# Performance work log

Measured on AMD Instinct MI355X. Metric: run time of the kernel, lower is better.

Reference implementation:

```python
import jax, jax.numpy as jnp
import numpy as np

N_LAYERS = 4
D = 512
H = 8
DH = D // H
DFF = 2048
VOCAB = 32000
SEQ_LEN = 512
MEM_LEN = 512
CMEM_LEN = 128
RATIO = 4
SCALE = DH ** -0.5


def _ln(x, g, b, eps=1e-5):
    mu = x.mean(-1, keepdims=True)
    var = ((x - mu) ** 2).mean(-1, keepdims=True)
    return (x - mu) * jax.lax.rsqrt(var + eps) * g + b


def _pe(t, d):
    # sinusoidal positional encoding buffer (PositionalEncoding)
    pos = np.arange(t, dtype=np.float32)[:, None]
    div = np.exp(np.arange(0, d, 2, dtype=np.float32) * (-np.log(10000.0) / d))
    pe = np.zeros((t, d), np.float32)
    pe[:, 0::2] = np.sin(pos * div)
    pe[:, 1::2] = np.cos(pos * div)
    return jnp.asarray(pe)


def _heads(x):  # [b,l,d] -> [b,h,l,dh]
    b, l, _ = x.shape
    return x.reshape(b, l, H, DH).transpose(0, 2, 1, 3)


def _full_attn(q, k, v):
    dots = jnp.einsum('bhid,bhjd->bhij', q, k) * SCALE
    return jnp.einsum('bhij,bhjd->bhid', jax.nn.softmax(dots, -1), v)


def _forward(seq, mask, mems, cmems, embed, ln1_g, ln1_b, Wq, Wkv, Wo, bo,
             conv_w, conv_b, ln2_g, ln2_b, W1, b1, W2, b2):
    b, t = seq.shape
    x = embed[seq] + _pe(t, D)[None]  # embedding + positional encoding
    # 2-D input mask -> [b,1,t,mem+cmem+t], True on memory positions
    mm = mask[:, None, :, None] & mask[:, None, None, :]
    full_mask = jnp.pad(mm, ((0, 0), (0, 0), (0, 0), (MEM_LEN + CMEM_LEN, 0)),
                        constant_values=True)
    neg = -jnp.finfo(jnp.float32).max
    new_mems, new_cmems, attns = [], [], []
    aux_total = jnp.zeros((), jnp.float32)
    for i in range(N_LAYERS):
        # PreNorm -> MemoryMultiHeadedAttention -> Residual
        xn = _ln(x, ln1_g[i], ln1_b[i])
        q = _heads(xn @ Wq[i])
        kv_in = jnp.concatenate([cmems[i], mems[i], xn], axis=1)  # [b,cm+m+t,d]
        k, v = jnp.split(kv_in @ Wkv[i], 2, axis=-1)
        k, v = _heads(k), _heads(v)
        dots = jnp.einsum('bhid,bhjd->bhij', q, k) * SCALE
        dots = jnp.where(full_mask, dots, neg)
        attn = jax.nn.softmax(dots, -1)
        out = jnp.einsum('bhij,bhjd->bhid', attn, v).transpose(0, 2, 1, 3).reshape(b, t, D)
        x = out @ Wo[i] + bo[i] + x  # to_out + residual
        # FIFO memory update: queue (mem, xn), keep last MEM_LEN
        queue = jnp.concatenate([mems[i], xn], axis=1)
        old_mem, new_mem = queue[:, :-MEM_LEN], queue[:, -MEM_LEN:]
        # ConvCompress with stride==kernel==RATIO -> non-overlapping blocks
        blocks = old_mem.reshape(b, -1, RATIO, D)
        compressed = jnp.einsum('birc,ocr->bio', blocks, conv_w[i]) + conv_b[i]
        new_cmem = jnp.concatenate([cmems[i], compressed], axis=1)[:, -CMEM_LEN:]
        # reconstruction attention loss; all operands detached as in source
        ck, cv = jnp.split(compressed @ Wkv[i], 2, axis=-1)
        qd, okd, ovd, ckd, cvd = map(jax.lax.stop_gradient, (
            q,
            k[:, :, CMEM_LEN:CMEM_LEN + MEM_LEN],
            v[:, :, CMEM_LEN:CMEM_LEN + MEM_LEN],
            _heads(ck), _heads(cv)))
        aux_total = aux_total + jnp.mean((_full_attn(qd, okd, ovd) - _full_attn(qd, ckd, cvd)) ** 2)
        # PreNorm -> FeedForward(GELU) -> Residual
        xn2 = _ln(x, ln2_g[i], ln2_b[i])
        x = x + jax.nn.gelu(xn2 @ W1[i] + b1[i], approximate=False) @ W2[i] + b2[i]
        new_mems.append(new_mem)
        new_cmems.append(new_cmem)
        attns.append(attn)
    attns_mean = jnp.mean(jnp.stack(attns), axis=(0, 1, 2))  # [t, cm+m+t]
    return (x, jnp.stack(new_mems), jnp.stack(new_cmems),
            aux_total / N_LAYERS, jnp.zeros((), jnp.float32), attns_mean)


def setup_inputs():
    key = jax.random.key(0)
    ks = jax.random.split(key, 12)
    s = 0.02
    return {
        'seq': jax.random.randint(ks[0], (8, SEQ_LEN), 0, VOCAB),
        'mask': jnp.ones((8, SEQ_LEN), bool),
        'mems': jax.random.normal(ks[1], (N_LAYERS, 8, MEM_LEN, D), jnp.float32) * s,
        'cmems': jax.random.normal(ks[2], (N_LAYERS, 8, CMEM_LEN, D), jnp.float32) * s,
        'embed': jax.random.normal(ks[3], (VOCAB, D), jnp.float32) * s,
        'ln1_g': jnp.ones((N_LAYERS, D)), 'ln1_b': jnp.zeros((N_LAYERS, D)),
        'Wq': jax.random.normal(ks[4], (N_LAYERS, D, D), jnp.float32) * s,
        'Wkv': jax.random.normal(ks[5], (N_LAYERS, D, 2 * D), jnp.float32) * s,
        'Wo': jax.random.normal(ks[6], (N_LAYERS, D, D), jnp.float32) * s,
        'bo': jnp.zeros((N_LAYERS, D)),
        'conv_w': jax.random.normal(ks[7], (N_LAYERS, D, D, RATIO), jnp.float32) * s,
        'conv_b': jnp.zeros((N_LAYERS, D)),
        'ln2_g': jnp.ones((N_LAYERS, D)), 'ln2_b': jnp.zeros((N_LAYERS, D)),
        'W1': jax.random.normal(ks[8], (N_LAYERS, D, DFF), jnp.float32) * s,
        'b1': jnp.zeros((N_LAYERS, DFF)),
        'W2': jax.random.normal(ks[9], (N_LAYERS, DFF, D), jnp.float32) * s,
        'b2': jnp.zeros((N_LAYERS, D)),
    }


def reference(seq, mask, mems, cmems, embed, ln1_g, ln1_b, Wq, Wkv, Wo, bo,
              conv_w, conv_b, ln2_g, ln2_b, W1, b1, W2, b2):
    return _forward(seq, mask, mems, cmems, embed, ln1_g, ln1_b, Wq, Wkv, Wo, bo,
                    conv_w, conv_b, ln2_g, ln2_b, W1, b1, W2, b2)
```

## Files before the change

### kernel.cpp

```cpp
#include <hip/hip_runtime.h>
#include <hip/hip_bf16.h>

#define DEV __device__ __forceinline__

typedef unsigned short u16;
typedef __attribute__((ext_vector_type(8))) short short8;
typedef __attribute__((ext_vector_type(4))) float floatx4;

DEV float gelu_f(float x){ return 0.5f*x*(1.0f+erff(x*0.7071067811865476f)); }

DEV u16 f2bf(float x){
  union { __hip_bfloat16 h; u16 u; } cv;
  cv.h = __float2bfloat16(x);
  return cv.u;
}
DEV float bf2f(u16 u){
  union { unsigned int u32; float f; } cv;
  cv.u32 = ((unsigned int)u) << 16;
  return cv.f;
}
DEV void split2(float v, u16* H, u16* L, long long i){
  u16 h = f2bf(v); H[i] = h; L[i] = f2bf(v - bf2f(h));
}

DEV void stage16(const u16* g, u16* lwave, int lane){
#if __has_builtin(__builtin_amdgcn_global_load_lds)
  __builtin_amdgcn_global_load_lds((const __attribute__((address_space(1))) void*)g,
                                   (__attribute__((address_space(3))) void*)lwave, 16, 0, 0);
#else
  *(short8*)(lwave + (long long)lane*8) = *(const short8*)g;
#endif
}

DEV float blockReduceSum(float v){
  __shared__ float red[4];
  int lane = threadIdx.x & 63, wid = threadIdx.x >> 6;
  #pragma unroll
  for (int off=32; off>0; off>>=1) v += __shfl_down(v, off, 64);
  __syncthreads();
  if (lane==0) red[wid]=v;
  __syncthreads();
  return red[0]+red[1]+red[2]+red[3];
}
DEV float blockReduceMax(float v){
  __shared__ float redm[4];
  int lane = threadIdx.x & 63, wid = threadIdx.x >> 6;
  #pragma unroll
  for (int off=32; off>0; off>>=1) v = fmaxf(v, __shfl_down(v, off, 64));
  __syncthreads();
  if (lane==0) redm[wid]=v;
  __syncthreads();
  return fmaxf(fmaxf(redm[0],redm[1]),fmaxf(redm[2],redm[3]));
}

template<int BM, int BN>
__global__ __launch_bounds__(256) void mgemm(
    const u16* __restrict__ AH, const u16* __restrict__ AL,
    const u16* __restrict__ BH, const u16* __restrict__ BL,
    float* __restrict__ C, u16* __restrict__ CH, u16* __restrict__ CL,
    const float* __restrict__ bias, const float* __restrict__ resid,
    float* __restrict__ mirror,
    int K, int lda, int ldb, int ldc,
    long long sA1, long long sA2, long long sB1, long long sB2,
    long long sC1, long long sC2, int B2, float scale, int act)
{
  const int b1 = blockIdx.z / B2, b2 = blockIdx.z % B2;
  const long long aOff = b1*sA1 + b2*sA2;
  const long long bOff = b1*sB1 + b2*sB2;
  const long long cOff = b1*sC1 + b2*sC2;
  AH += aOff; AL += aOff; BH += bOff; BL += bOff;
  if (C) C += cOff;
  if (CH){ CH += cOff; CL += cOff; }
  if (resid) resid += cOff;
  if (mirror) mirror += cOff;

  const int m0 = blockIdx.y*BM, n0 = blockIdx.x*BN;
  const int tid = threadIdx.x, lane = tid & 63, wid = tid >> 6;
  const int ln15 = lane & 15, quad = lane >> 4;
  constexpr int WM = BM/2, WN = BN/2, FM = WM/16, FN = WN/16;
  constexpr int RWA = BM/4, RWB = BN/4;
  constexpr int NIA = BM/64, NIB = BN/64;
  const int wr = wid >> 1, wc = wid & 1;

  __shared__ u16 AsH[2*BM*32];
  __shared__ u16 AsL[2*BM*32];
  __shared__ u16 BsH[2*BN*32];
  __shared__ u16 BsL[2*BN*32];

  floatx4 acc[FM][FN];
  #pragma unroll
  for (int a=0;a<FM;++a)
    #pragma unroll
    for (int b=0;b<FN;++b) acc[a][b] = (floatx4){0.f,0.f,0.f,0.f};

  const int rA = wid*RWA + (lane >> 2), cA = (lane & 3)*8;
  const int rB = wid*RWB + (lane >> 2), cB = (lane & 3)*8;
  const u16* pAH = AH + (long long)(m0 + rA)*lda + cA;
  const u16* pAL = AL + (long long)(m0 + rA)*lda + cA;
  const u16* pBH = BH + (long long)(n0 + rB)*ldb + cB;
  const u16* pBL = BL + (long long)(n0 + rB)*ldb + cB;
  u16* lAH = &AsH[wid*RWA*32];
  u16* lAL = &AsL[wid*RWA*32];
  u16* lBH = &BsH[wid*RWB*32];
  u16* lBL = &BsL[wid*RWB*32];

  for (int k0 = 0; k0 < K; k0 += 64) {
    #pragma unroll
    for (int s=0;s<2;++s){
      #pragma unroll
      for (int j=0;j<NIA;++j){
        stage16(pAH + s*32 + (long long)j*16*lda, lAH + s*BM*32 + j*512, lane);
        stage16(pAL + s*32 + (long long)j*16*lda, lAL + s*BM*32 + j*512, lane);
      }
      #pragma unroll
      for (int j=0;j<NIB;++j){
        stage16(pBH + s*32 + (long long)j*16*ldb, lBH + s*BN*32 + j*512, lane);
        stage16(pBL + s*32 + (long long)j*16*ldb, lBL + s*BN*32 + j*512, lane);
      }
    }
    __syncthreads();

    short8 ah[FM][2], al[FM][2], bh[FN][2], bl[FN][2];
    #pragma unroll
    for (int mi=0; mi<FM; ++mi)
      #pragma unroll
      for (int s=0;s<2;++s){
        const int off = s*BM*32 + (wr*WM + mi*16 + ln15)*32 + quad*8;
        ah[mi][s] = *(const short8*)&AsH[off];
        al[mi][s] = *(const short8*)&AsL[off];
      }
    #pragma unroll
    for (int ni=0; ni<FN; ++ni)
      #pragma unroll
      for (int s=0;s<2;++s){
        const int off = s*BN*32 + (wc*WN + ni*16 + ln15)*32 + quad*8;
        bh[ni][s] = *(const short8*)&BsH[off];
        bl[ni][s] = *(const short8*)&BsL[off];
      }
    #pragma unroll
    for (int mi=0; mi<FM; ++mi)
      #pragma unroll
      for (int ni=0; ni<FN; ++ni){
        floatx4 c = acc[mi][ni];
        #pragma unroll
        for (int s=0;s<2;++s){
          c = __builtin_amdgcn_mfma_f32_16x16x32_bf16(ah[mi][s], bh[ni][s], c, 0,0,0);
          c = __builtin_amdgcn_mfma_f32_16x16x32_bf16(ah[mi][s], bl[ni][s], c, 0,0,0);
          c = __builtin_amdgcn_mfma_f32_16x16x32_bf16(al[mi][s], bh[ni][s], c, 0,0,0);
        }
        acc[mi][ni] = c;
      }
    __syncthreads();
    pAH += 64; pAL += 64; pBH += 64; pBL += 64;
  }

  #pragma unroll
  for (int mi=0; mi<FM; ++mi){
    const int rb = m0 + wr*WM + mi*16 + quad*4;
    #pragma unroll
    for (int ni=0; ni<FN; ++ni){
      const int col = n0 + wc*WN + ni*16 + ln15;
      const float bv = bias ? bias[col] : 0.f;
      #pragma unroll
      for (int r=0; r<4; ++r){
        const long long ci = (long long)(rb+r)*ldc + col;
        float v = acc[mi][ni][r]*scale + bv;
        if (act==1) v = gelu_f(v);
        if (resid) v += resid[ci];
        if (C) C[ci] = v;
        if (CH){ u16 h=f2bf(v); CH[ci]=h; CL[ci]=f2bf(v-bf2f(h)); }
        if (mirror) mirror[ci] = v;
      }
    }
  }
}

__global__ __launch_bounds__(256) void wtrans_split(
    const float* __restrict__ W, u16* __restrict__ WTH, u16* __restrict__ WTL,
    int K, int N)
{
  __shared__ float t[32][33];
  const int k0 = blockIdx.x*32, n0 = blockIdx.y*32;
  const int r = threadIdx.x >> 5, c = threadIdx.x & 31;
  #pragma unroll
  for (int p=0;p<4;++p) t[r+p*8][c] = W[(long long)(k0+r+p*8)*N + n0+c];
  __syncthreads();
  #pragma unroll
  for (int p=0;p<4;++p){
    const float v = t[c][r+p*8];
    split2(v, WTH, WTL, (long long)(n0+r+p*8)*K + k0+c);
  }
}

__global__ __launch_bounds__(256) void wpermT_split(
    const float* __restrict__ w, u16* __restrict__ H, u16* __restrict__ L)
{
  const int idx = blockIdx.x*256 + threadIdx.x;
  const int o = idx >> 11, rem = idx & 2047;
  const int r = rem >> 9, c = rem & 511;
  split2(w[(long long)o*2048 + c*4 + r], H, L, idx);
}

__global__ __launch_bounds__(256) void vtrans_hl(
    const u16* __restrict__ kvH, const u16* __restrict__ kvL,
    u16* __restrict__ vTH, u16* __restrict__ vTL)
{
  const int z = blockIdx.y, t0 = blockIdx.x*64;
  const int b = z >> 3, h = z & 7;
  __shared__ u16 tH[64][72], tL[64][72];
  const int r = threadIdx.x >> 6, c = threadIdx.x & 63;
  #pragma unroll
  for (int p=0;p<16;++p){
    const int row = r + p*4;
    const long long off = (long long)b*1179648 + (long long)(t0+row)*1024 + 512 + h*64 + c;
    tH[row][c] = kvH[off];
    tL[row][c] = kvL[off];
  }
  __syncthreads();
  #pragma unroll
  for (int p=0;p<16;++p){
    const int d = r + p*4;
    const long long o = (long long)z*73728 + (long long)d*1152 + t0 + c;
    vTH[o] = tH[c][d];
    vTL[o] = tL[c][d];
  }
}

__global__ __launch_bounds__(256) void cvtrans_hl(
    const u16* __restrict__ ckvH, const u16* __restrict__ ckvL,
    u16* __restrict__ cvTH, u16* __restrict__ cvTL)
{
  const int z = blockIdx.y, t0 = blockIdx.x*64;
  const int b = z >> 3, h = z & 7;
  __shared__ u16 tH[64][72], tL[64][72];
  const int r = threadIdx.x >> 6, c = threadIdx.x & 63;
  #pragma unroll
  for (int p=0;p<16;++p){
    const int row = r + p*4;
    const long long off = (long long)b*131072 + (long long)(t0+row)*1024 + 512 + h*64 + c;
    tH[row][c] = ckvH[off];
    tL[row][c] = ckvL[off];
  }
  __syncthreads();
  #pragma unroll
  for (int p=0;p<16;++p){
    const int d = r + p*4;
    const long long o = (long long)z*8192 + (long long)d*128 + t0 + c;
    cvTH[o] = tH[c][d];
    cvTL[o] = tL[c][d];
  }
}

__global__ __launch_bounds__(256) void embed_kernel(
    const int* __restrict__ seq, const float* __restrict__ emb,
    float* __restrict__ x)
{
  const int row = blockIdx.x;
  const int t = row & 511;
  const long long tok = seq[row];
  #pragma unroll
  for (int p = 0; p < 2; ++p) {
    const int d = threadIdx.x + p*256;
    const int j2 = d & ~1;
    const float div = __expf((float)j2 * (-0.0179889460f));
    const float ang = (float)t * div;
    const float pe = (d & 1) ? cosf(ang) : sinf(ang);
    x[(long long)row*512 + d] = emb[tok*512 + d] + pe;
  }
}

__global__ __launch_bounds__(256) void ln_kernel(
    const float* __restrict__ x, const float* __restrict__ g,
    const float* __restrict__ b, u16* __restrict__ outH, u16* __restrict__ outL,
    float* __restrict__ mirror)
{
  const long long base = (long long)blockIdx.x*512;
  const int tid = threadIdx.x;
  const float v0 = x[base+tid], v1 = x[base+tid+256];
  const float mean = blockReduceSum(v0+v1) * (1.f/512.f);
  const float d0 = v0-mean, d1 = v1-mean;
  const float var = blockReduceSum(d0*d0+d1*d1) * (1.f/512.f);
  const float rstd = rsqrtf(var + 1e-5f);
  const float o0 = d0*rstd*g[tid]     + b[tid];
  const float o1 = d1*rstd*g[tid+256] + b[tid+256];
  split2(o0, outH, outL, base+tid);
  split2(o1, outH, outL, base+tid+256);
  if (mirror) { mirror[base+tid] = o0; mirror[base+tid+256] = o1; }
}

__global__ __launch_bounds__(256) void build_cm_kernel(
    const float* __restrict__ cmems_i, const float* __restrict__ mems_i,
    u16* __restrict__ H, u16* __restrict__ L)
{
  const long long idx = (long long)blockIdx.x*256 + threadIdx.x;
  const int c = (int)(idx & 511);
  const long long rb = idx >> 9;
  const int r = (int)(rb % 640);
  const int b = (int)(rb / 640);
  float v;
  if (r < 128) v = cmems_i[(long long)b*65536 + (long long)r*512 + c];
  else         v = mems_i[(long long)b*262144 + (long long)(r-128)*512 + c];
  split2(v, H, L, idx);
}

template<int MAXP>
__global__ __launch_bounds__(256) void softmax_hl(
    u16* __restrict__ H, u16* __restrict__ L, int Wd, float* __restrict__ acc)
{
  const long long base = (long long)blockIdx.x * Wd;
  float v[MAXP];
  float mx = -3.4e38f;
  #pragma unroll
  for (int p = 0; p < MAXP; ++p){
    const int i = threadIdx.x + p*256;
    v[p] = (i < Wd) ? bf2f(H[base+i]) + bf2f(L[base+i]) : -3.4e38f;
    mx = fmaxf(mx, v[p]);
  }
  mx = blockReduceMax(mx);
  float sum = 0.f;
  #pragma unroll
  for (int p = 0; p < MAXP; ++p){
    const int i = threadIdx.x + p*256;
    if (i < Wd){ v[p] = __expf(v[p] - mx); sum += v[p]; }
  }
  sum = blockReduceSum(sum);
  const float inv = 1.f/sum;
  float* arow = acc ? acc + (long long)(blockIdx.x & 511)*Wd : nullptr;
  #pragma unroll
  for (int p = 0; p < MAXP; ++p){
    const int i = threadIdx.x + p*256;
    if (i < Wd){
      const float e = v[p]*inv;
      split2(e, H, L, base+i);
      if (arow) atomicAdd(arow + i, e);
    }
  }
}

__global__ __launch_bounds__(256) void sqdiff_kernel(
    const float* __restrict__ a, const float* __restrict__ b, float* __restrict__ accum)
{
  const int idx0 = blockIdx.x*1024 + threadIdx.x;
  float s = 0.f;
  #pragma unroll
  for (int p = 0; p < 4; ++p) {
    const int idx = idx0 + p*256;
    const float d = a[idx]-b[idx];
    s += d*d;
  }
  s = blockReduceSum(s);
  if (threadIdx.x == 0) atomicAdd(accum, s);
}

__global__ __launch_bounds__(256) void attns_final_kernel(
    const float* __restrict__ asum, float* __restrict__ out)
{
  const int idx = blockIdx.x*256 + threadIdx.x;
  if (idx < 589824) out[idx] = asum[idx]*(1.f/256.f);
}

__global__ void aux_final_kernel(const float* __restrict__ aux, float* __restrict__ out)
{
  out[0] = aux[0] * (1.f/8388608.f);
  out[1] = 0.f;
}

extern "C" void kernel_launch(void* const* d_in, const int* in_sizes, int n_in,
                              void* d_out, int out_size, void* d_ws, size_t ws_size,
                              hipStream_t stream)
{
  const int*   seq    = (const int*)d_in[0];
  const float* mems   = (const float*)d_in[2];
  const float* cmems  = (const float*)d_in[3];
  const float* embed  = (const float*)d_in[4];
  const float* ln1_g  = (const float*)d_in[5];
  const float* ln1_b  = (const float*)d_in[6];
  const float* Wq     = (const float*)d_in[7];
  const float* Wkv    = (const float*)d_in[8];
  const float* Wo     = (const float*)d_in[9];
  const float* bo     = (const float*)d_in[10];
  const float* conv_w = (const float*)d_in[11];
  const float* conv_b = (const float*)d_in[12];
  const float* ln2_g  = (const float*)d_in[13];
  const float* ln2_b  = (const float*)d_in[14];
  const float* W1     = (const float*)d_in[15];
  const float* b1     = (const float*)d_in[16];
  const float* W2     = (const float*)d_in[17];
  const float* b2     = (const float*)d_in[18];
  float* out = (float*)d_out;

  char* W8 = (char*)d_ws;
  float* x     = (float*)(W8 + 0);
  u16* xnH     = (u16*)(W8 + 8388608LL);
  u16* xnL     = (u16*)(W8 + 12582912LL);
  u16* qH      = (u16*)(W8 + 16777216LL);
  u16* qL      = (u16*)(W8 + 20971520LL);
  u16* cmH     = (u16*)(W8 + 25165824LL);
  u16* cmL     = (u16*)(W8 + 30408704LL);
  u16* kvH     = (u16*)(W8 + 35651584LL);
  u16* kvL     = (u16*)(W8 + 54525952LL);
  u16* vTH     = (u16*)(W8 + 73400320LL);
  u16* vTL     = (u16*)(W8 + 82837504LL);
  u16* dotsH   = (u16*)(W8 + 92274688LL);
  u16* dotsL   = (u16*)(W8 + 111149056LL);
  u16* aoutH   = (u16*)(W8 + 130023424LL);
  u16* aoutL   = (u16*)(W8 + 134217728LL);
  u16* compH   = (u16*)(W8 + 138412032LL);
  u16* compL   = (u16*)(W8 + 139460608LL);
  u16* ckvH    = (u16*)(W8 + 140509184LL);
  u16* ckvL    = (u16*)(W8 + 142606336LL);
  u16* cvTH    = (u16*)(W8 + 144703488LL);
  u16* cvTL    = (u16*)(W8 + 145752064LL);
  u16* wpTH    = (u16*)(W8 + 146800640LL);
  u16* wpTL    = (u16*)(W8 + 148897792LL);
  u16* WqTH    = (u16*)(W8 + 150994944LL);
  u16* WqTL    = (u16*)(W8 + 151519232LL);
  u16* WkvTH   = (u16*)(W8 + 152043520LL);
  u16* WkvTL   = (u16*)(W8 + 153092096LL);
  u16* WoTH    = (u16*)(W8 + 154140672LL);
  u16* WoTL    = (u16*)(W8 + 154664960LL);
  u16* W1TH    = (u16*)(W8 + 155189248LL);
  u16* W1TL    = (u16*)(W8 + 157286400LL);
  u16* W2TH    = (u16*)(W8 + 159383552LL);
  u16* W2TL    = (u16*)(W8 + 161480704LL);
  float* o1    = (float*)(W8 + 163577856LL);
  float* o2    = (float*)(W8 + 171966464LL);
  float* attns = (float*)(W8 + 180355072LL);
  float* aux   = (float*)(W8 + 182714368LL);
  u16* xn2H = qH;  u16* xn2L = qL;
  u16* ffnhH = kvH; u16* ffnhL = kvL;

  hipMemsetAsync(attns, 0, 589824*sizeof(float), stream);
  hipMemsetAsync(aux, 0, sizeof(float), stream);

  embed_kernel<<<4096,256,0,stream>>>(seq, embed, x);

  for (int i = 0; i < 4; ++i) {
    const float* bo_i   = bo   + (long long)i*512;
    const float* cw_i   = conv_w + (long long)i*1048576;
    const float* cb_i   = conv_b + (long long)i*512;
    const float* b1_i   = b1   + (long long)i*2048;
    const float* b2_i   = b2   + (long long)i*512;
    const float* mems_i = mems + (long long)i*2097152;
    const float* cmems_i= cmems+ (long long)i*524288;
    float* out_mems_i   = out + 2097152LL  + (long long)i*2097152;
    float* out_cmems_i  = out + 10485760LL + (long long)i*524288;

    wtrans_split<<<dim3(16,16),256,0,stream>>>(Wq + (long long)i*262144,  WqTH, WqTL, 512, 512);
    wtrans_split<<<dim3(16,32),256,0,stream>>>(Wkv+ (long long)i*524288,  WkvTH,WkvTL,512, 1024);
    wtrans_split<<<dim3(16,16),256,0,stream>>>(Wo + (long long)i*262144,  WoTH, WoTL, 512, 512);
    wtrans_split<<<dim3(16,64),256,0,stream>>>(W1 + (long long)i*1048576, W1TH, W1TL, 512, 2048);
    wtrans_split<<<dim3(64,16),256,0,stream>>>(W2 + (long long)i*1048576, W2TH, W2TL, 2048,512);

    ln_kernel<<<4096,256,0,stream>>>(x, ln1_g+(long long)i*512, ln1_b+(long long)i*512, xnH, xnL, out_mems_i);
    mgemm<64,64><<<dim3(8,64,1),256,0,stream>>>(
        xnH,xnL, WqTH,WqTL, nullptr, qH,qL, nullptr,nullptr,nullptr,
        512, 512,512,512, 0,0,0,0,0,0, 1, 1.f, 0);
    build_cm_kernel<<<10240,256,0,stream>>>(cmems_i, mems_i, cmH, cmL);
    mgemm<64,128><<<dim3(8,10,8),256,0,stream>>>(
        cmH,cmL, WkvTH,WkvTL, nullptr, kvH,kvL, nullptr,nullptr,nullptr,
        512, 512,512,1024, 0,327680, 0,0, 0,1179648, 8, 1.f, 0);
    mgemm<64,128><<<dim3(8,8,8),256,0,stream>>>(
        xnH,xnL, WkvTH,WkvTL, nullptr, kvH+655360,kvL+655360, nullptr,nullptr,nullptr,
        512, 512,512,1024, 0,262144, 0,0, 0,1179648, 8, 1.f, 0);
    vtrans_hl<<<dim3(18,64),256,0,stream>>>(kvH, kvL, vTH, vTL);
    for (int c = 0; c < 4; ++c) {
      mgemm<64,128><<<dim3(9,8,16),256,0,stream>>>(
          qH + (long long)c*524288, qL + (long long)c*524288,
          kvH + (long long)c*2359296, kvL + (long long)c*2359296,
          nullptr, dotsH, dotsL, nullptr,nullptr,nullptr,
          64, 512,1024,1152, 262144,64, 1179648,64, 4718592,589824, 8, 0.125f, 0);
      softmax_hl<5><<<8192,256,0,stream>>>(dotsH, dotsL, 1152, attns);
      mgemm<64,64><<<dim3(1,8,16),256,0,stream>>>(
          dotsH, dotsL, vTH + (long long)c*1179648, vTL + (long long)c*1179648,
          nullptr, aoutH + (long long)c*524288, aoutL + (long long)c*524288,
          nullptr,nullptr,nullptr,
          1152, 1152,1152,512, 4718592,589824, 589824,73728, 262144,64, 8, 1.f, 0);
    }
    mgemm<64,64><<<dim3(8,64,1),256,0,stream>>>(
        aoutH,aoutL, WoTH,WoTL, x, nullptr,nullptr, bo_i, x, nullptr,
        512, 512,512,512, 0,0,0,0,0,0, 1, 1.f, 0);
    wpermT_split<<<4096,256,0,stream>>>(cw_i, wpTH, wpTL);
    mgemm<64,64><<<dim3(8,2,8),256,0,stream>>>(
        cmH+65536, cmL+65536, wpTH, wpTL, out_cmems_i, compH, compL, cb_i, nullptr, nullptr,
        2048, 2048,2048,512, 0,327680, 0,0, 0,65536, 8, 1.f, 0);
    mgemm<64,64><<<dim3(16,16,1),256,0,stream>>>(
        compH,compL, WkvTH,WkvTL, nullptr, ckvH,ckvL, nullptr,nullptr,nullptr,
        512, 512,512,1024, 0,0,0,0,0,0, 1, 1.f, 0);
    cvtrans_hl<<<dim3(2,64),256,0,stream>>>(ckvH, ckvL, cvTH, cvTL);
    for (int c = 0; c < 4; ++c) {
      mgemm<64,128><<<dim3(4,8,16),256,0,stream>>>(
          qH + (long long)c*524288, qL + (long long)c*524288,
          kvH + (long long)c*2359296 + 131072, kvL + (long long)c*2359296 + 131072,
          nullptr, dotsH, dotsL, nullptr,nullptr,nullptr,
          64, 512,1024,512, 262144,64, 1179648,64, 2097152,262144, 8, 0.125f, 0);
      softmax_hl<2><<<8192,256,0,stream>>>(dotsH, dotsL, 512, nullptr);
      mgemm<64,64><<<dim3(1,8,16),256,0,stream>>>(
          dotsH, dotsL, vTH + (long long)c*1179648 + 128, vTL + (long long)c*1179648 + 128,
          o1 + (long long)c*524288, nullptr,nullptr, nullptr,nullptr,nullptr,
          512, 512,1152,64, 2097152,262144, 589824,73728, 262144,32768, 8, 1.f, 0);
    }
    mgemm<64,128><<<dim3(1,8,64),256,0,stream>>>(
        qH,qL, ckvH,ckvL, nullptr, dotsH, dotsL, nullptr,nullptr,nullptr,
        64, 512,1024,128, 262144,64, 131072,64, 524288,65536, 8, 0.125f, 0);
    softmax_hl<1><<<32768,256,0,stream>>>(dotsH, dotsL, 128, nullptr);
    mgemm<64,64><<<dim3(1,8,64),256,0,stream>>>(
        dotsH, dotsL, cvTH, cvTL, o2, nullptr,nullptr, nullptr,nullptr,nullptr,
        128, 128,128,64, 524288,65536, 65536,8192, 262144,32768, 8, 1.f, 0);
    sqdiff_kernel<<<2048,256,0,stream>>>(o1, o2, aux);
    ln_kernel<<<4096,256,0,stream>>>(x, ln2_g+(long long)i*512, ln2_b+(long long)i*512, xn2H, xn2L, nullptr);
    mgemm<64,128><<<dim3(16,64,1),256,0,stream>>>(
        xn2H,xn2L, W1TH,W1TL, nullptr, ffnhH,ffnhL, b1_i, nullptr, nullptr,
        512, 512,512,2048, 0,0,0,0,0,0, 1, 1.f, 1);
    mgemm<64,64><<<dim3(8,64,1),256,0,stream>>>(
        ffnhH,ffnhL, W2TH,W2TL, x, nullptr,nullptr, b2_i, x, (i==3) ? out : nullptr,
        2048, 2048,2048,512, 0,0,0,0,0,0, 1, 1.f, 0);
  }

  attns_final_kernel<<<2304,256,0,stream>>>(attns, out + 12582914LL);
  aux_final_kernel<<<1,1,0,stream>>>(aux, out + 12582912LL);
}
```

Baseline: 3.539 ms.

## Fuse memory attention QK, softmax and PV into a two-pass flash kernel

Replaces the per-chunk sequence of QK^T GEMM, split-precision softmax and PV GEMM with a single fused attention kernel. A first pass computes running row max and sum over the 1152 keys; a second pass recomputes the scores, normalizes them, accumulates the attention map with atomics and multiplies by V from shared memory. This avoids writing and re-reading the large hi/lo score buffers and cuts several launches per layer. In exchange it computes QK twice and does many float atomicAdds into the attention map.

```diff
diff --git a/kernel.cpp b/kernel.cpp
--- a/kernel.cpp
+++ b/kernel.cpp
@@ -171,6 +171,201 @@
         if (CH){ u16 h=f2bf(v); CH[ci]=h; CL[ci]=f2bf(v-bf2f(h)); }
         if (mirror) mirror[ci] = v;
       }
+    }
+  }
+}
+
+__global__ __launch_bounds__(256) void fattn(
+    const u16* __restrict__ qH_, const u16* __restrict__ qL_,
+    const u16* __restrict__ kvH_, const u16* __restrict__ kvL_,
+    const u16* __restrict__ vTH_, const u16* __restrict__ vTL_,
+    u16* __restrict__ aoH, u16* __restrict__ aoL,
+    float* __restrict__ attns)
+{
+  const int z = blockIdx.y, b = z >> 3, h = z & 7;
+  const int t0 = blockIdx.x * 64;
+  const int tid = threadIdx.x, lane = tid & 63, wid = tid >> 6;
+  const int ln15 = lane & 15, quad = lane >> 4;
+
+  __shared__ u16 QsH[4096], QsL[4096], KsH[4096], KsL[4096];
+  __shared__ u16 VsH[4096], VsL[4096], PsH[4096], PsL[4096];
+
+  const int rS = wid*16 + (lane >> 2), cS = (lane & 3)*8;
+
+  {
+    const u16* qh = qH_ + (long long)(b*512 + t0 + rS)*512 + h*64 + cS;
+    const u16* ql = qL_ + (long long)(b*512 + t0 + rS)*512 + h*64 + cS;
+    stage16(qh,    &QsH[wid*512], lane);
+    stage16(qh+32, &QsH[2048 + wid*512], lane);
+    stage16(ql,    &QsL[wid*512], lane);
+    stage16(ql+32, &QsL[2048 + wid*512], lane);
+  }
+  const u16* kHb = kvH_ + (long long)b*1179648 + h*64;
+  const u16* kLb = kvL_ + (long long)b*1179648 + h*64;
+  const u16* vHb = vTH_ + (long long)z*73728;
+  const u16* vLb = vTL_ + (long long)z*73728;
+  __syncthreads();
+
+  short8 qfh[2], qfl[2];
+  #pragma unroll
+  for (int s=0;s<2;++s){
+    const int off = s*2048 + (wid*16 + ln15)*32 + quad*8;
+    qfh[s] = *(const short8*)&QsH[off];
+    qfl[s] = *(const short8*)&QsL[off];
+  }
+
+  float m_run[4] = {-3.4e38f,-3.4e38f,-3.4e38f,-3.4e38f};
+  float l_run[4] = {0.f,0.f,0.f,0.f};
+
+  for (int tt = 0; tt < 1152; tt += 64) {
+    __syncthreads();
+    {
+      const u16* kh = kHb + (long long)(tt + rS)*1024 + cS;
+      const u16* kl = kLb + (long long)(tt + rS)*1024 + cS;
+      stage16(kh,    &KsH[wid*512], lane);
+      stage16(kh+32, &KsH[2048 + wid*512], lane);
+      stage16(kl,    &KsL[wid*512], lane);
+      stage16(kl+32, &KsL[2048 + wid*512], lane);
+    }
+    __syncthreads();
+
+    short8 kh[4][2], kl[4][2];
+    #pragma unroll
+    for (int ni=0;ni<4;++ni)
+      #pragma unroll
+      for (int s=0;s<2;++s){
+        const int off = s*2048 + (ni*16 + ln15)*32 + quad*8;
+        kh[ni][s] = *(const short8*)&KsH[off];
+        kl[ni][s] = *(const short8*)&KsL[off];
+      }
+    floatx4 acc[4];
+    #pragma unroll
+    for (int ni=0;ni<4;++ni){
+      floatx4 c = (floatx4){0.f,0.f,0.f,0.f};
+      #pragma unroll
+      for (int s=0;s<2;++s){
+        c = __builtin_amdgcn_mfma_f32_16x16x32_bf16(qfh[s], kh[ni][s], c, 0,0,0);
+        c = __builtin_amdgcn_mfma_f32_16x16x32_bf16(qfh[s], kl[ni][s], c, 0,0,0);
+        c = __builtin_amdgcn_mfma_f32_16x16x32_bf16(qfl[s], kh[ni][s], c, 0,0,0);
+      }
+      acc[ni] = c;
+    }
+    #pragma unroll
+    for (int r=0;r<4;++r){
+      float v = fmaxf(fmaxf(acc[0][r],acc[1][r]),fmaxf(acc[2][r],acc[3][r]));
+      #pragma unroll
+      for (int o=1;o<16;o<<=1) v = fmaxf(v, __shfl_xor(v, o, 64));
+      const float mn = fmaxf(m_run[r], 0.125f*v);
+      float sum = 0.f;
+      #pragma unroll
+      for (int ni=0;ni<4;++ni) sum += __expf(0.125f*acc[ni][r] - mn);
+      #pragma unroll
+      for (int o=1;o<16;o<<=1) sum += __shfl_xor(sum, o, 64);
+      l_run[r] = l_run[r]*__expf(m_run[r]-mn) + sum;
+      m_run[r] = mn;
+    }
+  }
+  float invl[4];
+  #pragma unroll
+  for (int r=0;r<4;++r) invl[r] = 1.f/l_run[r];
+
+  floatx4 o_acc[4];
+  #pragma unroll
+  for (int ni=0;ni<4;++ni) o_acc[ni] = (floatx4){0.f,0.f,0.f,0.f};
+
+  for (int tt = 0; tt < 1152; tt += 64) {
+    __syncthreads();
+    {
+      const u16* kh = kHb + (long long)(tt + rS)*1024 + cS;
+      const u16* kl = kLb + (long long)(tt + rS)*1024 + cS;
+      stage16(kh,    &KsH[wid*512], lane);
+      stage16(kh+32, &KsH[2048 + wid*512], lane);
+      stage16(kl,    &KsL[wid*512], lane);
+      stage16(kl+32, &KsL[2048 + wid*512], lane);
+    }
+    __syncthreads();
+
+    short8 kh[4][2], kl[4][2];
+    #pragma unroll
+    for (int ni=0;ni<4;++ni)
+      #pragma unroll
+      for (int s=0;s<2;++s){
+        const int off = s*2048 + (ni*16 + ln15)*32 + quad*8;
+        kh[ni][s] = *(const short8*)&KsH[off];
+        kl[ni][s] = *(const short8*)&KsL[off];
+      }
+    floatx4 acc[4];
+    #pragma unroll
+    for (int ni=0;ni<4;++ni){
+      floatx4 c = (floatx4){0.f,0.f,0.f,0.f};
+      #pragma unroll
+      for (int s=0;s<2;++s){
+        c = __builtin_amdgcn_mfma_f32_16x16x32_bf16(qfh[s], kh[ni][s], c, 0,0,0);
+        c = __builtin_amdgcn_mfma_f32_16x16x32_bf16(qfh[s], kl[ni][s], c, 0,0,0);
+        c = __builtin_amdgcn_mfma_f32_16x16x32_bf16(qfl[s], kh[ni][s], c, 0,0,0);
+      }
+      acc[ni] = c;
+    }
+    const int rowl = wid*16 + quad*4;
+    #pragma unroll
+    for (int ni=0;ni<4;++ni){
+      const int cl = ln15 + ni*16;
+      const int soff = (cl>>5)*2048 + (cl&31);
+      #pragma unroll
+      for (int r=0;r<4;++r){
+        const float p = __expf(0.125f*acc[ni][r] - m_run[r])*invl[r];
+        atomicAdd(&attns[(long long)(t0 + rowl + r)*1152 + tt + cl], p);
+        const u16 hh = f2bf(p);
+        PsH[soff + (rowl+r)*32] = hh;
+        PsL[soff + (rowl+r)*32] = f2bf(p - bf2f(hh));
+      }
+    }
+    {
+      const u16* vh = vHb + (long long)rS*1152 + tt + cS;
+      const u16* vl = vLb + (long long)rS*1152 + tt + cS;
+      stage16(vh,    &VsH[wid*512], lane);
+      stage16(vh+32, &VsH[2048 + wid*512], lane);
+      stage16(vl,    &VsL[wid*512], lane);
+      stage16(vl+32, &VsL[2048 + wid*512], lane);
+    }
+    __syncthreads();
+
+    short8 pah[2], pal[2], vbh[4][2], vbl[4][2];
+    #pragma unroll
+    for (int s=0;s<2;++s){
+      const int off = s*2048 + (wid*16 + ln15)*32 + quad*8;
+      pah[s] = *(const short8*)&PsH[off];
+      pal[s] = *(const short8*)&PsL[off];
+    }
+    #pragma unroll
+    for (int ni=0;ni<4;++ni)
+      #pragma unroll
+      for (int s=0;s<2;++s){
+        const int off = s*2048 + (ni*16 + ln15)*32 + quad*8;
+        vbh[ni][s] = *(const short8*)&VsH[off];
+        vbl[ni][s] = *(const short8*)&VsL[off];
+      }
+    #pragma unroll
+    for (int ni=0;ni<4;++ni){
+      floatx4 c = o_acc[ni];
+      #pragma unroll
+      for (int s=0;s<2;++s){
+        c = __builtin_amdgcn_mfma_f32_16x16x32_bf16(pah[s], vbh[ni][s], c, 0,0,0);
+        c = __builtin_amdgcn_mfma_f32_16x16x32_bf16(pah[s], vbl[ni][s], c, 0,0,0);
+        c = __builtin_amdgcn_mfma_f32_16x16x32_bf16(pal[s], vbh[ni][s], c, 0,0,0);
+      }
+      o_acc[ni] = c;
+    }
+  }
+
+  const int rowl = wid*16 + quad*4;
+  #pragma unroll
+  for (int ni=0;ni<4;++ni){
+    const int col = h*64 + ln15 + ni*16;
+    #pragma unroll
+    for (int r=0;r<4;++r){
+      const long long ci = (long long)(b*512 + t0 + rowl + r)*512 + col;
+      split2(o_acc[ni][r], aoH, aoL, ci);
     }
   }
 }
@@ -464,19 +659,9 @@
         xnH,xnL, WkvTH,WkvTL, nullptr, kvH+655360,kvL+655360, nullptr,nullptr,nullptr,
         512, 512,512,1024, 0,262144, 0,0, 0,1179648, 8, 1.f, 0);
     vtrans_hl<<<dim3(18,64),256,0,stream>>>(kvH, kvL, vTH, vTL);
-    for (int c = 0; c < 4; ++c) {
-      mgemm<64,128><<<dim3(9,8,16),256,0,stream>>>(
-          qH + (long long)c*524288, qL + (long long)c*524288,
-          kvH + (long long)c*2359296, kvL + (long long)c*2359296,
-          nullptr, dotsH, dotsL, nullptr,nullptr,nullptr,
-          64, 512,1024,1152, 262144,64, 1179648,64, 4718592,589824, 8, 0.125f, 0);
-      softmax_hl<5><<<8192,256,0,stream>>>(dotsH, dotsL, 1152, attns);
-      mgemm<64,64><<<dim3(1,8,16),256,0,stream>>>(
-          dotsH, dotsL, vTH + (long long)c*1179648, vTL + (long long)c*1179648,
-          nullptr, aoutH + (long long)c*524288, aoutL + (long long)c*524288,
-          nullptr,nullptr,nullptr,
-          1152, 1152,1152,512, 4718592,589824, 589824,73728, 262144,64, 8, 1.f, 0);
-    }
+
+    fattn<<<dim3(8,64),256,0,stream>>>(qH,qL, kvH,kvL, vTH,vTL, aoutH,aoutL, attns);
+
     mgemm<64,64><<<dim3(8,64,1),256,0,stream>>>(
         aoutH,aoutL, WoTH,WoTL, x, nullptr,nullptr, bo_i, x, nullptr,
         512, 512,512,512, 0,0,0,0,0,0, 1, 1.f, 0);
```

New measurement: 2.984 ms. -15.7%, faster.
